# Kernel tuning notes

Hardware: AMD Instinct MI355X
Metric: run time of the kernel (lower is better)

## Reference

```python
import jax, jax.numpy as jnp
import numpy as np

DECAY = 0.9        # membrane leak factor per step (prms['decay'])
V_TH = 1.0         # spike threshold (prms['v_th'])
SUR_SCALE = 4.0    # surrogate-gradient sharpness (prms['surrogate_scale'])


def _spike(v):
    """Heaviside spike in forward; sigmoid surrogate in backward (straight-through)."""
    hard = (v >= V_TH).astype(v.dtype)
    sur = jax.nn.sigmoid(SUR_SCALE * (v - V_TH))
    return sur + jax.lax.stop_gradient(hard - sur)


def setup_inputs() -> dict:
    key = jax.random.key(0)
    k1, k2, k3 = jax.random.split(key, 3)
    B, T, P, D = 64, 256, 1024, 1024
    prv_voltage = jax.random.normal(k1, (B, T, P), dtype=jnp.float32)
    prv_spikes = (jax.random.uniform(k2, (B, T, P)) < 0.1).astype(jnp.float32)
    weights = jax.random.normal(k3, (P, D), dtype=jnp.float32) / np.float32(np.sqrt(P))
    return {"prv_voltage": prv_voltage, "prv_spikes": prv_spikes, "weights": weights}


def reference(prv_voltage, prv_spikes, weights):
    # synaptic currents for every step at once: (B, T, D)
    currents = jnp.einsum('btp,pd->btd', prv_spikes, weights)

    def step(v, i_t):
        v_new = DECAY * v + i_t            # leak + integrate
        s = _spike(v_new)                  # threshold
        v_next = v_new * (1.0 - s)         # reset-to-zero on spike
        return v_next, (v_new, s)

    B, T, D = currents.shape
    v0 = jnp.zeros((B, D), dtype=currents.dtype)
    _, (vs, ss) = jax.lax.scan(step, v0, jnp.swapaxes(currents, 0, 1))  # scan over time
    voltage = jnp.swapaxes(vs, 0, 1)  # (B, T, D)
    spikes = jnp.swapaxes(ss, 0, 1)   # (B, T, D)
    return voltage, spikes
```

## Files before the change

### kernel.cpp

```cpp
#include <hip/hip_runtime.h>


#define LIF_B 64
#define LIF_T 256
#define LIF_P 1024
#define LIF_D 1024
#define LIF_N ((size_t)LIF_B * LIF_T * LIF_D)

__global__ __launch_bounds__(256) void lif_currents_kernel(
    const float* __restrict__ spikes,
    const float* __restrict__ W,
    float* __restrict__ cur_out)
{
    const int row  = blockIdx.x;
    const int lane = threadIdx.x & 63;
    const int wave = threadIdx.x >> 6;
    const int dbase = wave << 8;

    const float* srow = spikes + (size_t)row * LIF_P;
    const float* wcol = W + dbase + (lane << 2);

    float a0x=0.f,a0y=0.f,a0z=0.f,a0w=0.f;
    float a1x=0.f,a1y=0.f,a1z=0.f,a1w=0.f;

    #define LIF_PANEL(J0, J1, AX, AY, AZ, AW)                                   \
    for (int j = (J0); j < (J1); ++j) {                                         \
        const float sv = srow[(j << 6) + lane];                                 \
        unsigned long long m = __ballot(sv != 0.0f);                            \
        const int pbase = j << 6;                                               \
        while (m) {                                                             \
            const int p = pbase + __builtin_ctzll(m);                           \
            m &= (m - 1);                                                       \
            const float4 wv =                                                   \
                *reinterpret_cast<const float4*>(wcol + ((size_t)p << 10));     \
            AX = __fadd_rn(AX, wv.x); AY = __fadd_rn(AY, wv.y);                 \
            AZ = __fadd_rn(AZ, wv.z); AW = __fadd_rn(AW, wv.w);                 \
        }                                                                       \
    }

    LIF_PANEL(0, 8,   a0x, a0y, a0z, a0w)
    LIF_PANEL(8, 16,  a1x, a1y, a1z, a1w)
    #undef LIF_PANEL

    float4 c;
    c.x = __fadd_rn(a0x, a1x);
    c.y = __fadd_rn(a0y, a1y);
    c.z = __fadd_rn(a0z, a1z);
    c.w = __fadd_rn(a0w, a1w);

    *reinterpret_cast<float4*>(cur_out + (size_t)row * LIF_D + dbase + (lane << 2)) = c;
}

__global__ __launch_bounds__(256) void lif_scan_kernel(
    float* __restrict__ voltage,
    float* __restrict__ spikes_out)
{
    const int tid = blockIdx.x * 256 + threadIdx.x;
    const int b = tid >> 10;
    const int d = tid & (LIF_D - 1);

    float v = 0.0f;
    const size_t base = ((size_t)b * LIF_T) * LIF_D + d;

    for (int t = 0; t < LIF_T; ++t) {
        const size_t idx = base + (size_t)t * LIF_D;
        const float cur = voltage[idx];
        const float vn = __fadd_rn(__fmul_rn(0.9f, v), cur);
        const bool fired = (vn >= 1.0f);
        voltage[idx]    = vn;
        spikes_out[idx] = fired ? 1.0f : 0.0f;
        v = fired ? 0.0f : vn;
    }
}

extern "C" void kernel_launch(void* const* d_in, const int* in_sizes, int n_in,
                              void* d_out, int out_size, void* d_ws, size_t ws_size,
                              hipStream_t stream) {
    (void)in_sizes; (void)n_in; (void)out_size; (void)d_ws; (void)ws_size;

    const float* spikes = (const float*)d_in[1];
    const float* W      = (const float*)d_in[2];

    float* out        = (float*)d_out;
    float* voltage    = out;
    float* spikes_out = out + LIF_N;

    lif_currents_kernel<<<LIF_B * LIF_T, 256, 0, stream>>>(spikes, W, voltage);
    lif_scan_kernel<<<(LIF_B * LIF_D) / 256, 256, 0, stream>>>(voltage, spikes_out);
}
```

Measured before the change: 310.7 us.

## Precompute spike index list in LDS and prefetch loads in LIF scan

```diff
diff --git a/kernel.cpp b/kernel.cpp
--- a/kernel.cpp
+++ b/kernel.cpp
@@ -12,35 +12,81 @@
     const float* __restrict__ W,
     float* __restrict__ cur_out)
 {
+    __shared__ unsigned long long smask[16];
+    __shared__ int plist[1024];
+    __shared__ int scnt[2];
+
     const int row  = blockIdx.x;
-    const int lane = threadIdx.x & 63;
-    const int wave = threadIdx.x >> 6;
+    const int tid  = threadIdx.x;
+    const int lane = tid & 63;
+    const int wave = tid >> 6;
     const int dbase = wave << 8;
 
     const float* srow = spikes + (size_t)row * LIF_P;
     const float* wcol = W + dbase + (lane << 2);
 
+    for (int jj = 0; jj < 4; ++jj) {
+        const int j = (wave << 2) + jj;
+        const float sv = srow[(j << 6) + lane];
+        const unsigned long long m = __ballot(sv != 0.0f);
+        if (lane == 0) smask[j] = m;
+    }
+    __syncthreads();
+
+    if (wave == 0) {
+        unsigned long long m = (lane < 16) ? smask[lane] : 0ULL;
+        const int pc = __popcll(m);
+        int s = pc;
+        for (int d = 1; d < 8; d <<= 1) {
+            const int vps = __shfl_up(s, d, 8);
+            if ((lane & 7) >= d) s += vps;
+        }
+        if (lane == 7)  scnt[0] = s;
+        if (lane == 15) scnt[1] = s;
+        if (lane < 16) {
+            int idx = ((lane < 8) ? 0 : 512) + (s - pc);
+            const int pb = lane << 6;
+            while (m) {
+                plist[idx++] = pb + __builtin_ctzll(m);
+                m &= (m - 1);
+            }
+        }
+    }
+    __syncthreads();
+
+    const int c0 = scnt[0];
+    const int c1 = scnt[1];
+
     float a0x=0.f,a0y=0.f,a0z=0.f,a0w=0.f;
     float a1x=0.f,a1y=0.f,a1z=0.f,a1w=0.f;
 
-    #define LIF_PANEL(J0, J1, AX, AY, AZ, AW)                                   \
-    for (int j = (J0); j < (J1); ++j) {                                         \
-        const float sv = srow[(j << 6) + lane];                                 \
-        unsigned long long m = __ballot(sv != 0.0f);                            \
-        const int pbase = j << 6;                                               \
-        while (m) {                                                             \
-            const int p = pbase + __builtin_ctzll(m);                           \
-            m &= (m - 1);                                                       \
-            const float4 wv =                                                   \
-                *reinterpret_cast<const float4*>(wcol + ((size_t)p << 10));     \
-            AX = __fadd_rn(AX, wv.x); AY = __fadd_rn(AY, wv.y);                 \
-            AZ = __fadd_rn(AZ, wv.z); AW = __fadd_rn(AW, wv.w);                 \
-        }                                                                       \
+    #define LIF_ACC(AX,AY,AZ,AW,WV)                                             \
+        AX = __fadd_rn(AX, (WV).x); AY = __fadd_rn(AY, (WV).y);                  \
+        AZ = __fadd_rn(AZ, (WV).z); AW = __fadd_rn(AW, (WV).w);
+
+    #define LIF_PANEL(BASE, CNT, AX,AY,AZ,AW)                                    \
+    {                                                                            \
+        int i = 0;                                                               \
+        for (; i + 4 <= (CNT); i += 4) {                                         \
+            const int4 ps = *reinterpret_cast<const int4*>(&plist[(BASE) + i]);  \
+            const float4 w0 = *reinterpret_cast<const float4*>(wcol + ((size_t)ps.x << 10)); \
+            const float4 w1 = *reinterpret_cast<const float4*>(wcol + ((size_t)ps.y << 10)); \
+            const float4 w2 = *reinterpret_cast<const float4*>(wcol + ((size_t)ps.z << 10)); \
+            const float4 w3 = *reinterpret_cast<const float4*>(wcol + ((size_t)ps.w << 10)); \
+            LIF_ACC(AX,AY,AZ,AW, w0) LIF_ACC(AX,AY,AZ,AW, w1)                    \
+            LIF_ACC(AX,AY,AZ,AW, w2) LIF_ACC(AX,AY,AZ,AW, w3)                    \
+        }                                                                        \
+        for (; i < (CNT); ++i) {                                                 \
+            const int p = plist[(BASE) + i];                                     \
+            const float4 wv = *reinterpret_cast<const float4*>(wcol + ((size_t)p << 10)); \
+            LIF_ACC(AX,AY,AZ,AW, wv)                                             \
+        }                                                                        \
     }
 
-    LIF_PANEL(0, 8,   a0x, a0y, a0z, a0w)
-    LIF_PANEL(8, 16,  a1x, a1y, a1z, a1w)
+    LIF_PANEL(0,   c0, a0x,a0y,a0z,a0w)
+    LIF_PANEL(512, c1, a1x,a1y,a1z,a1w)
     #undef LIF_PANEL
+    #undef LIF_ACC
 
     float4 c;
     c.x = __fadd_rn(a0x, a1x);
@@ -62,14 +108,48 @@
     float v = 0.0f;
     const size_t base = ((size_t)b * LIF_T) * LIF_D + d;
 
-    for (int t = 0; t < LIF_T; ++t) {
-        const size_t idx = base + (size_t)t * LIF_D;
-        const float cur = voltage[idx];
-        const float vn = __fadd_rn(__fmul_rn(0.9f, v), cur);
-        const bool fired = (vn >= 1.0f);
-        voltage[idx]    = vn;
-        spikes_out[idx] = fired ? 1.0f : 0.0f;
-        v = fired ? 0.0f : vn;
+    float p0 = voltage[base + 0*(size_t)LIF_D];
+    float p1 = voltage[base + 1*(size_t)LIF_D];
+    float p2 = voltage[base + 2*(size_t)LIF_D];
+    float p3 = voltage[base + 3*(size_t)LIF_D];
+
+    for (int t = 0; t < LIF_T; t += 4) {
+        const float c0 = p0, c1 = p1, c2 = p2, c3 = p3;
+        if (t + 4 < LIF_T) {
+            p0 = voltage[base + (size_t)(t + 4) * LIF_D];
+            p1 = voltage[base + (size_t)(t + 5) * LIF_D];
+            p2 = voltage[base + (size_t)(t + 6) * LIF_D];
+            p3 = voltage[base + (size_t)(t + 7) * LIF_D];
+        }
+        const size_t i0 = base + (size_t)t * LIF_D;
+        {
+            const float vn = __fadd_rn(__fmul_rn(0.9f, v), c0);
+            const bool f = (vn >= 1.0f);
+            voltage[i0 + 0*(size_t)LIF_D] = vn;
+            spikes_out[i0 + 0*(size_t)LIF_D] = f ? 1.0f : 0.0f;
+            v = f ? 0.0f : vn;
+        }
+        {
+            const float vn = __fadd_rn(__fmul_rn(0.9f, v), c1);
+            const bool f = (vn >= 1.0f);
+            voltage[i0 + 1*(size_t)LIF_D] = vn;
+            spikes_out[i0 + 1*(size_t)LIF_D] = f ? 1.0f : 0.0f;
+            v = f ? 0.0f : vn;
+        }
+        {
+            const float vn = __fadd_rn(__fmul_rn(0.9f, v), c2);
+            const bool f = (vn >= 1.0f);
+            voltage[i0 + 2*(size_t)LIF_D] = vn;
+            spikes_out[i0 + 2*(size_t)LIF_D] = f ? 1.0f : 0.0f;
+            v = f ? 0.0f : vn;
+        }
+        {
+            const float vn = __fadd_rn(__fmul_rn(0.9f, v), c3);
+            const bool f = (vn >= 1.0f);
+            voltage[i0 + 3*(size_t)LIF_D] = vn;
+            spikes_out[i0 + 3*(size_t)LIF_D] = f ? 1.0f : 0.0f;
+            v = f ? 0.0f : vn;
+        }
     }
 }
 
```

Result: faster. 272.1 us, median of 2 (-12.4%).
